# Kernel tuning notes

Hardware: AMD Instinct MI355X
Metric: run time of the kernel (lower is better)

Reference implementation:

```python
import jax, jax.numpy as jnp
import numpy as np

B, L, C = 32, 4096, 64
PL, PC = 64, 16          # patch sizes along L and C
NP = 256                 # num_patches
OUT = 512                # output_dim
FS = 1000.0              # sampling frequency -> T = 1/FS


def setup_inputs() -> dict:
    key = jax.random.key(0)
    ks = jax.random.split(key, 7)
    d_in = PL * (PC * 2)
    return {
        "x": jax.random.normal(ks[0], (B, L, C), dtype=jnp.float32),
        "start_L": jax.random.randint(ks[1], (B, NP), 0, L - PL + 1, dtype=jnp.int32),
        "start_C": jax.random.randint(ks[2], (B, NP), 0, C - PC + 1, dtype=jnp.int32),
        "w1": jax.random.normal(ks[3], (OUT, d_in), dtype=jnp.float32) / np.sqrt(d_in),
        "b1": jax.random.normal(ks[4], (OUT,), dtype=jnp.float32) * 0.01,
        "w2": jax.random.normal(ks[5], (OUT, OUT), dtype=jnp.float32) / np.sqrt(OUT),
        "b2": jax.random.normal(ks[6], (OUT,), dtype=jnp.float32) * 0.01,
    }


def reference(x, start_L, start_C, w1, b1, w2, b2):
    T = 1.0 / FS
    t = jnp.arange(L, dtype=jnp.float32) * T                      # [L]

    # patch index grids (wrapping, as in the torch module)
    idx_L = (start_L[:, :, None] + jnp.arange(PL, dtype=jnp.int32)) % L   # [B,NP,PL]
    idx_C = (start_C[:, :, None] + jnp.arange(PC, dtype=jnp.int32)) % C   # [B,NP,PC]

    # double gather: patches[b,p,i,j] = x[b, idx_L[b,p,i], idx_C[b,p,j]]
    b_idx = jnp.arange(B, dtype=jnp.int32)[:, None, None, None]
    patches = x[b_idx, idx_L[:, :, :, None], idx_C[:, :, None, :]]        # [B,NP,PL,PC]

    # time embedding gathered with the same L indices, broadcast over PC
    t_patches = jnp.broadcast_to(t[idx_L][:, :, :, None], (B, NP, PL, PC))

    feats = jnp.concatenate([patches, t_patches], axis=-1)                # [B,NP,PL,2*PC]
    feats = feats.reshape(B, NP, PL * 2 * PC)

    h = jnp.einsum('bpd,od->bpo', feats, w1) + b1
    h = jax.nn.silu(h)
    out = jnp.einsum('bpo,qo->bpq', h, w2) + b2                           # [B,NP,OUT]
    return out
```

## Files before the change

### kernel.cpp

```cpp
#include <hip/hip_runtime.h>
#include <hip/hip_bf16.h>
#include <stdint.h>

#define LL   4096
#define CCH  64
#define DOUT 512
#define MM   8192
#define TT   0.001f

using bf16 = __hip_bfloat16;
typedef __attribute__((ext_vector_type(8))) short bf16x8;
typedef __attribute__((ext_vector_type(4))) float f32x4;

__device__ __forceinline__ uint2 pack4_bf16(float a, float b, float c, float d) {
    union { bf16 h[4]; uint2 u; } p;
    p.h[0] = __float2bfloat16(a);
    p.h[1] = __float2bfloat16(b);
    p.h[2] = __float2bfloat16(c);
    p.h[3] = __float2bfloat16(d);
    return p.u;
}

__global__ __launch_bounds__(256) void prep(
    const float* __restrict__ w1, const float* __restrict__ b1,
    const float* __restrict__ w2,
    bf16* __restrict__ w1g, bf16* __restrict__ w2g,
    float* __restrict__ A1, float* __restrict__ C1)
{
    const int blk = blockIdx.x;
    if (blk < 512) {
        int g   = blk * 256 + threadIdx.x;
        int kk0 = (g & 7) * 4;
        int col = (g >> 3) & 511;
        int ic  = g >> 12;
        int l   = ic * 2 + (kk0 >> 4);
        int j0  = kk0 & 15;
        float4 v = *(const float4*)(w1 + (size_t)col * 2048 + l * 32 + j0);
        *(uint2*)(w1g + ((size_t)(ic * 512 + col) * 32 + kk0)) =
            pack4_bf16(v.x, v.y, v.z, v.w);
    } else if (blk < 768) {
        int g   = (blk - 512) * 256 + threadIdx.x;
        int kk0 = (g & 7) * 4;
        int col = (g >> 3) & 511;
        int ic2 = g >> 12;
        float4 v = *(const float4*)(w2 + (size_t)col * 512 + ic2 * 32 + kk0);
        *(uint2*)(w2g + ((size_t)(ic2 * 512 + col) * 32 + kk0)) =
            pack4_bf16(v.x, v.y, v.z, v.w);
    } else {
        const int o = (blk - 768) * 4 + (threadIdx.x >> 6);
        const int l = threadIdx.x & 63;
        const float* wr = w1 + (size_t)o * 2048 + l * 32 + 16;
        float s0 = 0.f;
#pragma unroll
        for (int j = 0; j < 16; ++j) s0 += wr[j];
        float s1 = (float)l * s0;
#pragma unroll
        for (int off = 32; off > 0; off >>= 1) {
            s0 += __shfl_down(s0, off);
            s1 += __shfl_down(s1, off);
        }
        if (l == 0) {
            A1[o] = TT * s0;
            C1[o] = b1[o] + TT * s1;
        }
    }
}

__global__ __launch_bounds__(512, 2) void mega(
    const float* __restrict__ x, const int* __restrict__ sLg,
    const int* __restrict__ sCg, const bf16* __restrict__ w1g,
    const bf16* __restrict__ w2g, const float* __restrict__ A1,
    const float* __restrict__ C1, const float* __restrict__ b2,
    float* __restrict__ out)
{
    __shared__ __align__(16) bf16 Asm[32 * 1024];
    bf16* const Hs = Asm;

    const int t    = threadIdx.x;
    const int lane = t & 63;
    const int wave = t >> 6;
    const int fr   = lane & 15;
    const int fq   = lane >> 4;
    const int m0   = blockIdx.x * 32;
    const int b    = m0 >> 8;

    {
        const int gr  = t >> 4;
        const int gs  = t & 15;
        const int gsl = sLg[m0 + gr];
        const int gsc = sCg[m0 + gr];
        const float* gx = x + ((size_t)b * LL + gsl + (gs >> 2)) * CCH
                            + gsc + (gs & 3) * 4;
        float4 xv[16];
#pragma unroll
        for (int p = 0; p < 16; ++p)
            xv[p] = *(const float4*)(gx + (size_t)p * 4 * CCH);
#pragma unroll
        for (int p = 0; p < 16; ++p) {
            const int l = 4 * p + (gs >> 2);
            const int u = l * 2 + ((gs & 3) >> 1);
            const int idx = gr * 1024 + ((u ^ (gr & 7)) * 8) + (gs & 1) * 4;
            *(uint2*)(Asm + idx) = pack4_bf16(xv[p].x, xv[p].y, xv[p].z, xv[p].w);
        }
    }
    __syncthreads();

    const bf16* const w1base = w1g + (size_t)(wave * 64 + fr) * 32 + fq * 8;
    f32x4 acc[2][4] = {};
    {
        bf16x8 bnx[4];
#pragma unroll
        for (int j = 0; j < 4; ++j)
            bnx[j] = *(const bf16x8*)(w1base + j * 512);
#pragma unroll
        for (int it = 0; it < 32; ++it) {
            bf16x8 bcur[4];
#pragma unroll
            for (int j = 0; j < 4; ++j) bcur[j] = bnx[j];
            if (it < 31) {
                const bf16* p = w1base + (size_t)(it + 1) * 16384;
#pragma unroll
                for (int j = 0; j < 4; ++j)
                    bnx[j] = *(const bf16x8*)(p + j * 512);
            }
            bf16x8 af[2];
#pragma unroll
            for (int i = 0; i < 2; ++i) {
                const int row = i * 16 + fr;
                const int u   = it * 4 + fq;
                af[i] = *(const bf16x8*)&Asm[row * 1024 + ((u ^ (row & 7)) * 8)];
            }
#pragma unroll
            for (int i = 0; i < 2; ++i)
#pragma unroll
                for (int j = 0; j < 4; ++j)
                    acc[i][j] = __builtin_amdgcn_mfma_f32_16x16x32_bf16(
                        af[i], bcur[j], acc[i][j], 0, 0, 0);
        }
    }
    __syncthreads();

    {
        float slr[2][4];
#pragma unroll
        for (int i = 0; i < 2; ++i)
#pragma unroll
            for (int rr = 0; rr < 4; ++rr)
                slr[i][rr] = (float)sLg[m0 + i * 16 + fq * 4 + rr];
#pragma unroll
        for (int j = 0; j < 4; ++j) {
            const int col = wave * 64 + j * 16 + fr;
            const float av = A1[col];
            const float cv = C1[col];
            const int c8 = col >> 3, c7 = col & 7;
#pragma unroll
            for (int i = 0; i < 2; ++i)
#pragma unroll
                for (int rr = 0; rr < 4; ++rr) {
                    const int row = i * 16 + fq * 4 + rr;
                    float v = acc[i][j][rr] + slr[i][rr] * av + cv;
                    v = v / (1.0f + __expf(-v));
                    Hs[row * 512 + ((c8 ^ (row & 7)) * 8) + c7] = __float2bfloat16(v);
                }
        }
    }
    __syncthreads();

    const bf16* const w2base = w2g + (size_t)(wave * 64 + fr) * 32 + fq * 8;
    f32x4 acc2[2][4] = {};
    {
        bf16x8 bnx[4];
#pragma unroll
        for (int j = 0; j < 4; ++j)
            bnx[j] = *(const bf16x8*)(w2base + j * 512);
#pragma unroll
        for (int it2 = 0; it2 < 16; ++it2) {
            bf16x8 bcur[4];
#pragma unroll
            for (int j = 0; j < 4; ++j) bcur[j] = bnx[j];
            if (it2 < 15) {
                const bf16* p = w2base + (size_t)(it2 + 1) * 16384;
#pragma unroll
                for (int j = 0; j < 4; ++j)
                    bnx[j] = *(const bf16x8*)(p + j * 512);
            }
            bf16x8 af[2];
#pragma unroll
            for (int i = 0; i < 2; ++i) {
                const int row = i * 16 + fr;
                const int u2  = it2 * 4 + fq;
                af[i] = *(const bf16x8*)&Hs[row * 512 + ((u2 ^ (row & 7)) * 8)];
            }
#pragma unroll
            for (int i = 0; i < 2; ++i)
#pragma unroll
                for (int j = 0; j < 4; ++j)
                    acc2[i][j] = __builtin_amdgcn_mfma_f32_16x16x32_bf16(
                        af[i], bcur[j], acc2[i][j], 0, 0, 0);
        }
    }

#pragma unroll
    for (int j = 0; j < 4; ++j) {
        const int col = wave * 64 + j * 16 + fr;
        const float bv = b2[col];
#pragma unroll
        for (int i = 0; i < 2; ++i)
#pragma unroll
            for (int rr = 0; rr < 4; ++rr) {
                const int row = m0 + i * 16 + fq * 4 + rr;
                out[(size_t)row * 512 + col] = acc2[i][j][rr] + bv;
            }
    }
}

extern "C" void kernel_launch(void* const* d_in, const int* in_sizes, int n_in,
                              void* d_out, int out_size, void* d_ws, size_t ws_size,
                              hipStream_t stream)
{
    const float* x  = (const float*)d_in[0];
    const int*   sL = (const int*)  d_in[1];
    const int*   sC = (const int*)  d_in[2];
    const float* w1 = (const float*)d_in[3];
    const float* b1 = (const float*)d_in[4];
    const float* w2 = (const float*)d_in[5];
    const float* b2 = (const float*)d_in[6];
    float* out = (float*)d_out;

    char* ws = (char*)d_ws;
    bf16*  w1g = (bf16*)ws;
    bf16*  w2g = (bf16*)(ws + (1 << 20));
    float* A1  = (float*)(ws + (1 << 20) + (1 << 19));
    float* C1  = A1 + DOUT;

    prep<<<896, 256, 0, stream>>>(w1, b1, w2, w1g, w2g, A1, C1);
    mega<<<MM / 32, 512, 0, stream>>>(x, sL, sC, w1g, w2g, A1, C1, b2, out);
}
```

Baseline: 123.8 us.

## Split fused kernel into gather and two weight-stationary GEMM kernels

Replaces the single fused kernel with three kernels. The first gathers the patches into a bf16 global buffer. The second runs GEMM1 with a 64-column slice of W1 held in LDS through async global-to-LDS copies while A fragments stream from global, then applies SiLU and writes H as bf16 to global memory. The third runs GEMM2 the same way and writes the output with nontemporal stores. The aim is to stop every block re-streaming the full weight matrices, at the cost of extra launches and a global round trip for the features and H.

```diff
diff --git a/kernel.cpp b/kernel.cpp
--- a/kernel.cpp
+++ b/kernel.cpp
@@ -11,6 +11,15 @@
 using bf16 = __hip_bfloat16;
 typedef __attribute__((ext_vector_type(8))) short bf16x8;
 typedef __attribute__((ext_vector_type(4))) float f32x4;
+
+#define MFMA(a, b, c) __builtin_amdgcn_mfma_f32_16x16x32_bf16((a), (b), (c), 0, 0, 0)
+
+__device__ __forceinline__ void async_copy16(void* lds, const void* g) {
+    __builtin_amdgcn_global_load_lds(
+        (const __attribute__((address_space(1))) void*)g,
+        (__attribute__((address_space(3))) void*)lds,
+        16, 0, 0);
+}
 
 __device__ __forceinline__ uint2 pack4_bf16(float a, float b, float c, float d) {
     union { bf16 h[4]; uint2 u; } p;
@@ -66,151 +75,205 @@
     }
 }
 
-__global__ __launch_bounds__(512, 2) void mega(
-    const float* __restrict__ x, const int* __restrict__ sLg,
-    const int* __restrict__ sCg, const bf16* __restrict__ w1g,
-    const bf16* __restrict__ w2g, const float* __restrict__ A1,
-    const float* __restrict__ C1, const float* __restrict__ b2,
-    float* __restrict__ out)
-{
-    __shared__ __align__(16) bf16 Asm[32 * 1024];
-    bf16* const Hs = Asm;
-
+__global__ __launch_bounds__(256) void gather(
+    const float* __restrict__ x, const int* __restrict__ sL,
+    const int* __restrict__ sC, bf16* __restrict__ fg)
+{
+    const int g  = blockIdx.x * 256 + threadIdx.x;
+    const int ic = g >> 13;
+    const int m  = g & 8191;
+    const int b  = m >> 8;
+    const int sl = sL[m];
+    const int sc = sC[m];
+    const float* p = x + ((size_t)b * LL + sl + ic * 2) * CCH + sc;
+    float4 v0 = *(const float4*)(p);
+    float4 v1 = *(const float4*)(p + 4);
+    float4 v2 = *(const float4*)(p + 8);
+    float4 v3 = *(const float4*)(p + 12);
+    float4 u0 = *(const float4*)(p + CCH);
+    float4 u1 = *(const float4*)(p + CCH + 4);
+    float4 u2 = *(const float4*)(p + CCH + 8);
+    float4 u3 = *(const float4*)(p + CCH + 12);
+    bf16* dst = fg + ((size_t)ic * MM + m) * 32;
+    uint4 o;
+    uint2 a, c;
+    a = pack4_bf16(v0.x, v0.y, v0.z, v0.w);
+    c = pack4_bf16(v1.x, v1.y, v1.z, v1.w);
+    o.x = a.x; o.y = a.y; o.z = c.x; o.w = c.y;  *(uint4*)(dst)      = o;
+    a = pack4_bf16(v2.x, v2.y, v2.z, v2.w);
+    c = pack4_bf16(v3.x, v3.y, v3.z, v3.w);
+    o.x = a.x; o.y = a.y; o.z = c.x; o.w = c.y;  *(uint4*)(dst + 8)  = o;
+    a = pack4_bf16(u0.x, u0.y, u0.z, u0.w);
+    c = pack4_bf16(u1.x, u1.y, u1.z, u1.w);
+    o.x = a.x; o.y = a.y; o.z = c.x; o.w = c.y;  *(uint4*)(dst + 16) = o;
+    a = pack4_bf16(u2.x, u2.y, u2.z, u2.w);
+    c = pack4_bf16(u3.x, u3.y, u3.z, u3.w);
+    o.x = a.x; o.y = a.y; o.z = c.x; o.w = c.y;  *(uint4*)(dst + 24) = o;
+}
+
+__global__ __launch_bounds__(512, 2) void gemm1_inv(
+    const bf16* __restrict__ fg, const bf16* __restrict__ w1g,
+    const float* __restrict__ A1, const float* __restrict__ C1,
+    const int* __restrict__ sLg, bf16* __restrict__ hg)
+{
+    __shared__ __align__(16) bf16 Bs[32 * 64 * 32];
     const int t    = threadIdx.x;
     const int lane = t & 63;
     const int wave = t >> 6;
     const int fr   = lane & 15;
     const int fq   = lane >> 4;
-    const int m0   = blockIdx.x * 32;
-    const int b    = m0 >> 8;
-
-    {
-        const int gr  = t >> 4;
-        const int gs  = t & 15;
-        const int gsl = sLg[m0 + gr];
-        const int gsc = sCg[m0 + gr];
-        const float* gx = x + ((size_t)b * LL + gsl + (gs >> 2)) * CCH
-                            + gsc + (gs & 3) * 4;
-        float4 xv[16];
-#pragma unroll
-        for (int p = 0; p < 16; ++p)
-            xv[p] = *(const float4*)(gx + (size_t)p * 4 * CCH);
-#pragma unroll
-        for (int p = 0; p < 16; ++p) {
-            const int l = 4 * p + (gs >> 2);
-            const int u = l * 2 + ((gs & 3) >> 1);
-            const int idx = gr * 1024 + ((u ^ (gr & 7)) * 8) + (gs & 1) * 4;
-            *(uint2*)(Asm + idx) = pack4_bf16(xv[p].x, xv[p].y, xv[p].z, xv[p].w);
-        }
-    }
+    const int r0   = blockIdx.x * 256;
+    const int n0   = blockIdx.y * 64;
+
+    const bf16* const w1s = w1g + (size_t)lane * 8;
+#pragma unroll
+    for (int s = 0; s < 4; ++s) {
+        const int ic = wave + s * 8;
+#pragma unroll
+        for (int q = 0; q < 4; ++q)
+            async_copy16(&Bs[(ic * 64 + q * 16) * 32],
+                         w1s + ((size_t)ic * 512 + n0 + q * 16) * 32);
+    }
+
+    const bf16* ab = fg + ((size_t)(r0 + wave * 32 + fr)) * 32 + fq * 8;
+    bf16x8 aA[2], aB[2];
+    aA[0] = *(const bf16x8*)(ab);
+    aA[1] = *(const bf16x8*)(ab + 16 * 32);
+    aB[0] = *(const bf16x8*)(ab + (size_t)MM * 32);
+    aB[1] = *(const bf16x8*)(ab + (size_t)MM * 32 + 16 * 32);
     __syncthreads();
 
-    const bf16* const w1base = w1g + (size_t)(wave * 64 + fr) * 32 + fq * 8;
     f32x4 acc[2][4] = {};
-    {
-        bf16x8 bnx[4];
-#pragma unroll
-        for (int j = 0; j < 4; ++j)
-            bnx[j] = *(const bf16x8*)(w1base + j * 512);
-#pragma unroll
-        for (int it = 0; it < 32; ++it) {
-            bf16x8 bcur[4];
-#pragma unroll
-            for (int j = 0; j < 4; ++j) bcur[j] = bnx[j];
-            if (it < 31) {
-                const bf16* p = w1base + (size_t)(it + 1) * 16384;
-#pragma unroll
-                for (int j = 0; j < 4; ++j)
-                    bnx[j] = *(const bf16x8*)(p + j * 512);
-            }
-            bf16x8 af[2];
-#pragma unroll
-            for (int i = 0; i < 2; ++i) {
-                const int row = i * 16 + fr;
-                const int u   = it * 4 + fq;
-                af[i] = *(const bf16x8*)&Asm[row * 1024 + ((u ^ (row & 7)) * 8)];
-            }
-#pragma unroll
-            for (int i = 0; i < 2; ++i)
-#pragma unroll
-                for (int j = 0; j < 4; ++j)
-                    acc[i][j] = __builtin_amdgcn_mfma_f32_16x16x32_bf16(
-                        af[i], bcur[j], acc[i][j], 0, 0, 0);
-        }
-    }
+#pragma unroll
+    for (int it = 0; it < 16; ++it) {
+        {
+            const int ic = 2 * it;
+            bf16x8 bfrg[4];
+#pragma unroll
+            for (int j = 0; j < 4; ++j)
+                bfrg[j] = *(const bf16x8*)&Bs[(ic * 64 + j * 16 + fr) * 32 + fq * 8];
+#pragma unroll
+            for (int j = 0; j < 4; ++j) {
+                acc[0][j] = MFMA(aA[0], bfrg[j], acc[0][j]);
+                acc[1][j] = MFMA(aA[1], bfrg[j], acc[1][j]);
+            }
+            if (it < 15) {
+                const bf16* p = ab + (size_t)(ic + 2) * MM * 32;
+                aA[0] = *(const bf16x8*)(p);
+                aA[1] = *(const bf16x8*)(p + 16 * 32);
+            }
+        }
+        {
+            const int ic = 2 * it + 1;
+            bf16x8 bfrg[4];
+#pragma unroll
+            for (int j = 0; j < 4; ++j)
+                bfrg[j] = *(const bf16x8*)&Bs[(ic * 64 + j * 16 + fr) * 32 + fq * 8];
+#pragma unroll
+            for (int j = 0; j < 4; ++j) {
+                acc[0][j] = MFMA(aB[0], bfrg[j], acc[0][j]);
+                acc[1][j] = MFMA(aB[1], bfrg[j], acc[1][j]);
+            }
+            if (it < 15) {
+                const bf16* p = ab + (size_t)(ic + 2) * MM * 32;
+                aB[0] = *(const bf16x8*)(p);
+                aB[1] = *(const bf16x8*)(p + 16 * 32);
+            }
+        }
+    }
+
+    float slr[2][4];
+#pragma unroll
+    for (int i = 0; i < 2; ++i)
+#pragma unroll
+        for (int rr = 0; rr < 4; ++rr)
+            slr[i][rr] = (float)sLg[r0 + wave * 32 + i * 16 + fq * 4 + rr];
+#pragma unroll
+    for (int j = 0; j < 4; ++j) {
+        const int col = n0 + j * 16 + fr;
+        const float av = A1[col];
+        const float cv = C1[col];
+        const int icg = (n0 >> 5) + (j >> 1);
+        const int kc  = (j & 1) * 16 + fr;
+#pragma unroll
+        for (int i = 0; i < 2; ++i)
+#pragma unroll
+            for (int rr = 0; rr < 4; ++rr) {
+                const int row = r0 + wave * 32 + i * 16 + fq * 4 + rr;
+                float v = acc[i][j][rr] + slr[i][rr] * av + cv;
+                v = v / (1.0f + __expf(-v));
+                hg[((size_t)icg * MM + row) * 32 + kc] = __float2bfloat16(v);
+            }
+    }
+}
+
+__global__ __launch_bounds__(512, 4) void gemm2_inv(
+    const bf16* __restrict__ hg, const bf16* __restrict__ w2g,
+    const float* __restrict__ b2, float* __restrict__ out)
+{
+    __shared__ __align__(16) bf16 Bs[16 * 64 * 32];
+    const int t    = threadIdx.x;
+    const int lane = t & 63;
+    const int wave = t >> 6;
+    const int fr   = lane & 15;
+    const int fq   = lane >> 4;
+    const int r0   = blockIdx.x * 128;
+    const int n0   = blockIdx.y * 64;
+
+    const bf16* const w2s = w2g + (size_t)lane * 8;
+#pragma unroll
+    for (int s = 0; s < 2; ++s) {
+        const int ic = wave + s * 8;
+#pragma unroll
+        for (int q = 0; q < 4; ++q)
+            async_copy16(&Bs[(ic * 64 + q * 16) * 32],
+                         w2s + ((size_t)ic * 512 + n0 + q * 16) * 32);
+    }
+
+    const bf16* ab = hg + ((size_t)(r0 + wave * 16 + fr)) * 32 + fq * 8;
+    bf16x8 aA = *(const bf16x8*)(ab);
+    bf16x8 aB = *(const bf16x8*)(ab + (size_t)MM * 32);
     __syncthreads();
 
-    {
-        float slr[2][4];
-#pragma unroll
-        for (int i = 0; i < 2; ++i)
-#pragma unroll
-            for (int rr = 0; rr < 4; ++rr)
-                slr[i][rr] = (float)sLg[m0 + i * 16 + fq * 4 + rr];
-#pragma unroll
-        for (int j = 0; j < 4; ++j) {
-            const int col = wave * 64 + j * 16 + fr;
-            const float av = A1[col];
-            const float cv = C1[col];
-            const int c8 = col >> 3, c7 = col & 7;
-#pragma unroll
-            for (int i = 0; i < 2; ++i)
-#pragma unroll
-                for (int rr = 0; rr < 4; ++rr) {
-                    const int row = i * 16 + fq * 4 + rr;
-                    float v = acc[i][j][rr] + slr[i][rr] * av + cv;
-                    v = v / (1.0f + __expf(-v));
-                    Hs[row * 512 + ((c8 ^ (row & 7)) * 8) + c7] = __float2bfloat16(v);
-                }
-        }
-    }
-    __syncthreads();
-
-    const bf16* const w2base = w2g + (size_t)(wave * 64 + fr) * 32 + fq * 8;
-    f32x4 acc2[2][4] = {};
-    {
-        bf16x8 bnx[4];
-#pragma unroll
-        for (int j = 0; j < 4; ++j)
-            bnx[j] = *(const bf16x8*)(w2base + j * 512);
-#pragma unroll
-        for (int it2 = 0; it2 < 16; ++it2) {
-            bf16x8 bcur[4];
-#pragma unroll
-            for (int j = 0; j < 4; ++j) bcur[j] = bnx[j];
-            if (it2 < 15) {
-                const bf16* p = w2base + (size_t)(it2 + 1) * 16384;
-#pragma unroll
-                for (int j = 0; j < 4; ++j)
-                    bnx[j] = *(const bf16x8*)(p + j * 512);
-            }
-            bf16x8 af[2];
-#pragma unroll
-            for (int i = 0; i < 2; ++i) {
-                const int row = i * 16 + fr;
-                const int u2  = it2 * 4 + fq;
-                af[i] = *(const bf16x8*)&Hs[row * 512 + ((u2 ^ (row & 7)) * 8)];
-            }
-#pragma unroll
-            for (int i = 0; i < 2; ++i)
-#pragma unroll
-                for (int j = 0; j < 4; ++j)
-                    acc2[i][j] = __builtin_amdgcn_mfma_f32_16x16x32_bf16(
-                        af[i], bcur[j], acc2[i][j], 0, 0, 0);
+    f32x4 acc[4] = {};
+#pragma unroll
+    for (int it = 0; it < 8; ++it) {
+        {
+            const int ic = 2 * it;
+            bf16x8 bfrg[4];
+#pragma unroll
+            for (int j = 0; j < 4; ++j)
+                bfrg[j] = *(const bf16x8*)&Bs[(ic * 64 + j * 16 + fr) * 32 + fq * 8];
+#pragma unroll
+            for (int j = 0; j < 4; ++j)
+                acc[j] = MFMA(aA, bfrg[j], acc[j]);
+            if (it < 7)
+                aA = *(const bf16x8*)(ab + (size_t)(ic + 2) * MM * 32);
+        }
+        {
+            const int ic = 2 * it + 1;
+            bf16x8 bfrg[4];
+#pragma unroll
+            for (int j = 0; j < 4; ++j)
+                bfrg[j] = *(const bf16x8*)&Bs[(ic * 64 + j * 16 + fr) * 32 + fq * 8];
+#pragma unroll
+            for (int j = 0; j < 4; ++j)
+                acc[j] = MFMA(aB, bfrg[j], acc[j]);
+            if (it < 7)
+                aB = *(const bf16x8*)(ab + (size_t)(ic + 2) * MM * 32);
         }
     }
 
 #pragma unroll
     for (int j = 0; j < 4; ++j) {
-        const int col = wave * 64 + j * 16 + fr;
+        const int col = n0 + j * 16 + fr;
         const float bv = b2[col];
 #pragma unroll
-        for (int i = 0; i < 2; ++i)
-#pragma unroll
-            for (int rr = 0; rr < 4; ++rr) {
-                const int row = m0 + i * 16 + fq * 4 + rr;
-                out[(size_t)row * 512 + col] = acc2[i][j][rr] + bv;
-            }
+        for (int rr = 0; rr < 4; ++rr) {
+            const int row = r0 + wave * 16 + fq * 4 + rr;
+            __builtin_nontemporal_store(acc[j][rr] + bv,
+                                        out + (size_t)row * 512 + col);
+        }
     }
 }
 
@@ -232,7 +295,11 @@
     bf16*  w2g = (bf16*)(ws + (1 << 20));
     float* A1  = (float*)(ws + (1 << 20) + (1 << 19));
     float* C1  = A1 + DOUT;
+    bf16*  fg  = (bf16*)(ws + (2 << 20));
+    bf16*  hg  = (bf16*)(ws + (2 << 20) + ((size_t)MM * 1024 * 2));
 
     prep<<<896, 256, 0, stream>>>(w1, b1, w2, w1g, w2g, A1, C1);
-    mega<<<MM / 32, 512, 0, stream>>>(x, sL, sC, w1g, w2g, A1, C1, b2, out);
-}
+    gather<<<1024, 256, 0, stream>>>(x, sL, sC, fg);
+    gemm1_inv<<<dim3(32, 8), 512, 0, stream>>>(fg, w1g, A1, C1, sL, hg);
+    gemm2_inv<<<dim3(64, 8), 512, 0, stream>>>(hg, w2g, b2, out);
+}
```

After: 128.8 us. 4.0% more time.
